# Kernel optimization log

Hardware: AMD Instinct MI355X
Metric: run time of the kernel (lower is better)

The kernel has to match this reference:

```python
import jax, jax.numpy as jnp
import numpy as np

N, E = 50000, 800000
F_IN, H, C = 128, 4, 32
NEG_SLOPE = 0.2

def setup_inputs() -> dict:
    key = jax.random.key(0)
    k1, k2, k3, k4, k5, k6 = jax.random.split(key, 6)
    x = jax.random.normal(k1, (N, F_IN), dtype=jnp.float32)
    edge_index = jax.random.randint(k2, (2, E), 0, N, dtype=jnp.int64)
    # GATConv params: lin weight [F_IN, H*C], att_src/att_dst [H, C], bias [H*C]
    W = jax.random.normal(k3, (F_IN, H * C), dtype=jnp.float32) * (1.0 / np.sqrt(F_IN))
    att_src = jax.random.normal(k4, (H, C), dtype=jnp.float32) * (1.0 / np.sqrt(C))
    att_dst = jax.random.normal(k5, (H, C), dtype=jnp.float32) * (1.0 / np.sqrt(C))
    bias = jax.random.normal(k6, (H * C,), dtype=jnp.float32) * 0.01
    return {"x": x, "edge_index": edge_index, "W": W, "att_src": att_src, "att_dst": att_dst, "bias": bias}

def reference(x, edge_index, W, att_src, att_dst, bias):
    # Linear transform: [N, H, C]
    h = (x @ W).reshape(N, H, C)
    # Per-node attention logits: [N, H]
    a_src = jnp.einsum('nhc,hc->nh', h, att_src)
    a_dst = jnp.einsum('nhc,hc->nh', h, att_dst)
    # PyG GATConv adds self-loops by default
    loop = jnp.arange(N, dtype=edge_index.dtype)
    src = jnp.concatenate([edge_index[0], loop])  # message source j
    dst = jnp.concatenate([edge_index[1], loop])  # message target i
    # Edge logits + LeakyReLU: [E+N, H]
    e = jax.nn.leaky_relu(a_src[src] + a_dst[dst], NEG_SLOPE)
    # Segment softmax over incoming edges per target node
    m = jax.ops.segment_max(e, dst, num_segments=N)  # [N, H]
    e_exp = jnp.exp(e - m[dst])
    denom = jax.ops.segment_sum(e_exp, dst, num_segments=N)  # [N, H]
    att = e_exp / denom[dst]  # [E+N, H]
    # Scatter-add weighted messages: [N, H, C]
    out = jax.ops.segment_sum(h[src] * att[:, :, None], dst, num_segments=N)
    return out.reshape(N, H * C) + bias
```

## Files before the change

### kernel.cpp

```cpp
#include <hip/hip_runtime.h>
#include <cstdint>

#define NNODES 50000
#define NEDGES 800000
#define NEG 0.2f
#define NBKT 196
#define BCAP 5120

typedef __attribute__((ext_vector_type(8))) short short8;
typedef __attribute__((ext_vector_type(4))) float f32x4;

#define AS_STRIDE 136
#define CS_STRIDE 132

__device__ __forceinline__ float leaky(float v) { return v > 0.f ? v : NEG * v; }

__device__ __forceinline__ unsigned short f2bf(float f) {
    unsigned int u = __float_as_uint(f);
    u += 0x7fff + ((u >> 16) & 1);
    return (unsigned short)(u >> 16);
}

__device__ __forceinline__ int block_excl_scan(int v, int t) {
    __shared__ int wsum[4];
    const int lane = t & 63, wv = t >> 6;
    int x = v;
    #pragma unroll
    for (int m = 1; m < 64; m <<= 1) {
        int u = __shfl_up(x, m);
        if (lane >= m) x += u;
    }
    if (lane == 63) wsum[wv] = x;
    __syncthreads();
    if (t == 0) {
        int run = 0;
        #pragma unroll
        for (int i = 0; i < 4; ++i) { int tmp = wsum[i]; wsum[i] = run; run += tmp; }
    }
    __syncthreads();
    return x - v + wsum[wv];
}

__global__ __launch_bounds__(256) void gemm_k(const float* __restrict__ x,
                                              const float* __restrict__ W,
                                              unsigned short* __restrict__ hb,
                                              const float* __restrict__ att_src,
                                              const float* __restrict__ att_dst,
                                              float* __restrict__ a_src,
                                              float* __restrict__ a_dst) {
    __shared__ __align__(16) char smem[52224];
    unsigned short* As = (unsigned short*)smem;
    unsigned short* Bs = (unsigned short*)(smem + 17408);
    float*          Cs = (float*)smem;

    const int tid = threadIdx.x;
    const int rbase = blockIdx.x * 64;

    #pragma unroll
    for (int i = 0; i < 8; ++i) {
        int f = tid + i * 256;
        int r = f >> 5, c4 = (f & 31) * 4;
        float4 xv = make_float4(0.f, 0.f, 0.f, 0.f);
        if (rbase + r < NNODES) xv = ((const float4*)x)[(size_t)(rbase + r) * 32 + (f & 31)];
        unsigned int p0 = ((unsigned int)f2bf(xv.y) << 16) | f2bf(xv.x);
        unsigned int p1 = ((unsigned int)f2bf(xv.w) << 16) | f2bf(xv.z);
        *(uint2*)(As + r * AS_STRIDE + c4) = make_uint2(p0, p1);
    }
    #pragma unroll
    for (int i = 0; i < 64; ++i) {
        int f = tid + i * 256;
        int k = f >> 7, n = f & 127;
        Bs[n * AS_STRIDE + k] = f2bf(W[f]);
    }
    __syncthreads();

    const int lane = tid & 63, w = tid >> 6;
    const int quad = lane >> 4, m16 = lane & 15;

    short8 af[4];
    #pragma unroll
    for (int s = 0; s < 4; ++s)
        af[s] = *(const short8*)(As + (w * 16 + m16) * AS_STRIDE + s * 32 + quad * 8);

    f32x4 acc[8];
    #pragma unroll
    for (int t = 0; t < 8; ++t) acc[t] = (f32x4){0.f, 0.f, 0.f, 0.f};

    #pragma unroll
    for (int t = 0; t < 8; ++t) {
        #pragma unroll
        for (int s = 0; s < 4; ++s) {
            short8 bf = *(const short8*)(Bs + (t * 16 + m16) * AS_STRIDE + s * 32 + quad * 8);
            acc[t] = __builtin_amdgcn_mfma_f32_16x16x32_bf16(af[s], bf, acc[t], 0, 0, 0);
        }
    }
    __syncthreads();

    #pragma unroll
    for (int t = 0; t < 8; ++t)
        #pragma unroll
        for (int r = 0; r < 4; ++r)
            Cs[(w * 16 + quad * 4 + r) * CS_STRIDE + t * 16 + m16] = acc[t][r];
    __syncthreads();

    const int cp = lane;
    float2 as_v = ((const float2*)att_src)[cp];
    float2 ad_v = ((const float2*)att_dst)[cp];
    #pragma unroll
    for (int r = 0; r < 16; ++r) {
        int row = w * 16 + r;
        int row_g = rbase + row;
        float2 cv = *(const float2*)(Cs + row * CS_STRIDE + 2 * cp);
        ushort2 hs;
        hs.x = f2bf(cv.x); hs.y = f2bf(cv.y);
        if (row_g < NNODES) ((ushort2*)(hb + (size_t)row_g * 128))[cp] = hs;
        float ps = cv.x * as_v.x + cv.y * as_v.y;
        float pd = cv.x * ad_v.x + cv.y * ad_v.y;
        #pragma unroll
        for (int m = 8; m >= 1; m >>= 1) {
            ps += __shfl_xor(ps, m, 16);
            pd += __shfl_xor(pd, m, 16);
        }
        if (row_g < NNODES && (cp & 15) == 0) {
            a_src[row_g * 4 + (cp >> 4)] = ps;
            a_dst[row_g * 4 + (cp >> 4)] = pd;
        }
    }
}

__global__ __launch_bounds__(256) void bin_k(const int* __restrict__ ei,
                                             int* __restrict__ bcnt,
                                             unsigned int* __restrict__ bktdata) {
    __shared__ int lhist[NBKT];
    __shared__ int lofs[NBKT];
    __shared__ int lcur[NBKT];
    __shared__ int gbase[NBKT];
    __shared__ unsigned int staged[4096];
    const int b = blockIdx.x, t = threadIdx.x;
    for (int i = t; i < NBKT; i += 256) lhist[i] = 0;
    __syncthreads();
    unsigned int pk[16];
    int bk[16];
    const int e0 = b * 4096;
    #pragma unroll
    for (int i = 0; i < 16; ++i) {
        int e = e0 + i * 256 + t;
        if (e < NEDGES) {
            int s = ei[e], d = ei[NEDGES + e];
            bk[i] = d >> 8;
            pk[i] = ((unsigned)bk[i] << 24) | ((unsigned)(d & 255) << 16) | (unsigned)s;
            atomicAdd(&lhist[bk[i]], 1);
        } else bk[i] = -1;
    }
    __syncthreads();
    int v = (t < NBKT) ? lhist[t] : 0;
    int excl = block_excl_scan(v, t);
    if (t < NBKT) { lofs[t] = excl; lcur[t] = excl; }
    __syncthreads();
    if (t < NBKT) gbase[t] = (v > 0) ? atomicAdd(&bcnt[t], v) : 0;
    #pragma unroll
    for (int i = 0; i < 16; ++i) {
        if (bk[i] >= 0) {
            int pos = atomicAdd(&lcur[bk[i]], 1);
            staged[pos] = pk[i];
        }
    }
    __syncthreads();
    const int total = lofs[NBKT - 1] + lhist[NBKT - 1];
    for (int i = t; i < total; i += 256) {
        unsigned int ent = staged[i];
        int bb = ent >> 24;
        int pos = gbase[bb] + (i - lofs[bb]);
        bktdata[(size_t)bb * BCAP + pos] = ent & 0x00FFFFFFu;
    }
}

__global__ __launch_bounds__(256) void bscan_k(const int* __restrict__ bcnt,
                                               int* __restrict__ bktoff) {
    const int t = threadIdx.x;
    int v = (t < NBKT) ? bcnt[t] : 0;
    int excl = block_excl_scan(v, t);
    if (t < NBKT) bktoff[t] = excl;
}

__global__ __launch_bounds__(256) void sort_k(const int* __restrict__ bcnt,
                                              const int* __restrict__ bktoff,
                                              const unsigned int* __restrict__ bktdata,
                                              int* __restrict__ off,
                                              int* __restrict__ csr) {
    __shared__ unsigned int staged[BCAP];
    __shared__ int sorted[BCAP];
    __shared__ int lcnt[256];
    __shared__ int lcur[256];
    const int b = blockIdx.x, t = threadIdx.x;
    const int cnt = bcnt[b], base = bktoff[b];
    lcnt[t] = 0;
    for (int i = t; i < cnt; i += 256) staged[i] = bktdata[(size_t)b * BCAP + i];
    __syncthreads();
    for (int i = t; i < cnt; i += 256) atomicAdd(&lcnt[staged[i] >> 16], 1);
    __syncthreads();
    int v = lcnt[t];
    int excl = block_excl_scan(v, t);
    lcur[t] = excl;
    const int node = b * 256 + t;
    if (node <= NNODES) off[node] = base + excl;
    __syncthreads();
    for (int i = t; i < cnt; i += 256) {
        unsigned int ent = staged[i];
        int pos = atomicAdd(&lcur[ent >> 16], 1);
        sorted[pos] = (int)(ent & 0xFFFFu);
    }
    __syncthreads();
    for (int i = t; i < cnt; i += 256) csr[base + i] = sorted[i];
}

__global__ __launch_bounds__(256) void gather_k(const int* __restrict__ off,
                                                const int* __restrict__ csr,
                                                const unsigned short* __restrict__ hb,
                                                const float* __restrict__ a_src,
                                                const float* __restrict__ a_dst,
                                                const float* __restrict__ bias,
                                                float* __restrict__ out) {
    const int wid = threadIdx.x >> 6, lane = threadIdx.x & 63;
    const int n = blockIdx.x * 4 + wid;
    if (n >= NNODES) return;
    const int head = lane >> 4;
    const int sub  = lane & 15;
    const int g = head, q = sub;
    const int head_c = q >> 2;

    const float a_d = a_dst[n * 4 + head];
    float acc[8];
    #pragma unroll
    for (int k = 0; k < 8; ++k) acc[k] = 0.f;

    if (g == 0) {
        float wsc = __expf(leaky(a_src[n * 4 + head_c] + a_dst[n * 4 + head_c]));
        uint4 hv = ((const uint4*)(hb + (size_t)n * 128))[q];
        acc[0] = wsc * __uint_as_float(hv.x << 16);
        acc[1] = wsc * __uint_as_float(hv.x & 0xffff0000u);
        acc[2] = wsc * __uint_as_float(hv.y << 16);
        acc[3] = wsc * __uint_as_float(hv.y & 0xffff0000u);
        acc[4] = wsc * __uint_as_float(hv.z << 16);
        acc[5] = wsc * __uint_as_float(hv.z & 0xffff0000u);
        acc[6] = wsc * __uint_as_float(hv.w << 16);
        acc[7] = wsc * __uint_as_float(hv.w & 0xffff0000u);
    }
    float denom = (sub == 0) ? __expf(leaky(a_src[n * 4 + head] + a_d)) : 0.f;

    const int beg = off[n], end = off[n + 1];
    for (int base = beg; base < end; base += 16) {
        int m = end - base; if (m > 16) m = 16;
        int s = 0;
        float w = 0.f;
        if (sub < m) {
            s = csr[base + sub];
            w = __expf(leaky(a_src[s * 4 + head] + a_d));
        }
        denom += w;
        #pragma unroll
        for (int jj = 0; jj < 4; ++jj) {
            int j = jj * 4 + g;
            int   sj = __shfl(s, j);
            float wj = __shfl(w, (head_c << 4) | j);
            if (j < m) {
                uint4 hv = ((const uint4*)(hb + (size_t)sj * 128))[q];
                acc[0] += wj * __uint_as_float(hv.x << 16);
                acc[1] += wj * __uint_as_float(hv.x & 0xffff0000u);
                acc[2] += wj * __uint_as_float(hv.y << 16);
                acc[3] += wj * __uint_as_float(hv.y & 0xffff0000u);
                acc[4] += wj * __uint_as_float(hv.z << 16);
                acc[5] += wj * __uint_as_float(hv.z & 0xffff0000u);
                acc[6] += wj * __uint_as_float(hv.w << 16);
                acc[7] += wj * __uint_as_float(hv.w & 0xffff0000u);
            }
        }
    }
    #pragma unroll
    for (int mm = 8; mm >= 1; mm >>= 1) denom += __shfl_xor(denom, mm, 16);
    const float inv = __frcp_rn(__shfl(denom, head_c << 4));
    #pragma unroll
    for (int k = 0; k < 8; ++k) {
        acc[k] += __shfl_xor(acc[k], 16);
        acc[k] += __shfl_xor(acc[k], 32);
    }
    if (g == 0) {
        float4 b0 = ((const float4*)bias)[2 * q];
        float4 b1 = ((const float4*)bias)[2 * q + 1];
        float4* orow = (float4*)(out + (size_t)n * 128);
        orow[2 * q]     = make_float4(acc[0] * inv + b0.x, acc[1] * inv + b0.y,
                                      acc[2] * inv + b0.z, acc[3] * inv + b0.w);
        orow[2 * q + 1] = make_float4(acc[4] * inv + b1.x, acc[5] * inv + b1.y,
                                      acc[6] * inv + b1.z, acc[7] * inv + b1.w);
    }
}

extern "C" void kernel_launch(void* const* d_in, const int* in_sizes, int n_in,
                              void* d_out, int out_size, void* d_ws, size_t ws_size,
                              hipStream_t stream) {
    const float* x     = (const float*)d_in[0];
    const int*   ei    = (const int*)d_in[1];
    const float* W     = (const float*)d_in[2];
    const float* att_s = (const float*)d_in[3];
    const float* att_d = (const float*)d_in[4];
    const float* bias  = (const float*)d_in[5];
    float*       out   = (float*)d_out;
    char*        ws    = (char*)d_ws;

    unsigned short* hb = (unsigned short*)(ws);
    float* a_src  = (float*)(ws + 12800000);
    float* a_dst  = (float*)(ws + 13600000);
    int*   off    = (int*)  (ws + 14400000);
    int*   csr    = (int*)  (ws + 14600768);
    unsigned int* bktdata = (unsigned int*)(ws + 17800768);
    int*   bcnt   = (int*)  (ws + 21814848);
    int*   bktoff = (int*)  (ws + 21815680);

    hipMemsetAsync(bcnt, 0, NBKT * sizeof(int), stream);
    gemm_k  <<<782,   256, 0, stream>>>(x, W, hb, att_s, att_d, a_src, a_dst);
    bin_k   <<<196,   256, 0, stream>>>(ei, bcnt, bktdata);
    bscan_k <<<1,     256, 0, stream>>>(bcnt, bktoff);
    sort_k  <<<196,   256, 0, stream>>>(bcnt, bktoff, bktdata, off, csr);
    gather_k<<<12500, 256, 0, stream>>>(off, csr, hb, a_src, a_dst, bias, out);
}
```

Baseline: 170.1 us.

## Merge GEMM and edge binning into one launch, fold bucket scan into sort

The GEMM and edge-binning kernels become a single launch whose blocks branch on block index, so the two independent stages run concurrently. The single-block bucket scan kernel is removed and each sort block recomputes the 196-entry prefix scan itself. The W load is also vectorised to float4. Together this cuts two kernel launches and the serialization between them. In exchange, binning blocks now reserve the GEMM's large shared allocation, which may lower their occupancy.

```diff
diff --git a/kernel.cpp b/kernel.cpp
--- a/kernel.cpp
+++ b/kernel.cpp
@@ -6,6 +6,7 @@
 #define NEG 0.2f
 #define NBKT 196
 #define BCAP 5120
+#define GEMM_BLOCKS 782
 
 typedef __attribute__((ext_vector_type(8))) short short8;
 typedef __attribute__((ext_vector_type(4))) float f32x4;
@@ -41,150 +42,146 @@
     return x - v + wsum[wv];
 }
 
-__global__ __launch_bounds__(256) void gemm_k(const float* __restrict__ x,
-                                              const float* __restrict__ W,
-                                              unsigned short* __restrict__ hb,
-                                              const float* __restrict__ att_src,
-                                              const float* __restrict__ att_dst,
-                                              float* __restrict__ a_src,
-                                              float* __restrict__ a_dst) {
+__global__ __launch_bounds__(256) void fused_k(const float* __restrict__ x,
+                                               const float* __restrict__ W,
+                                               unsigned short* __restrict__ hb,
+                                               const float* __restrict__ att_src,
+                                               const float* __restrict__ att_dst,
+                                               float* __restrict__ a_src,
+                                               float* __restrict__ a_dst,
+                                               const int* __restrict__ ei,
+                                               int* __restrict__ bcnt,
+                                               unsigned int* __restrict__ bktdata) {
     __shared__ __align__(16) char smem[52224];
-    unsigned short* As = (unsigned short*)smem;
-    unsigned short* Bs = (unsigned short*)(smem + 17408);
-    float*          Cs = (float*)smem;
-
     const int tid = threadIdx.x;
-    const int rbase = blockIdx.x * 64;
-
-    #pragma unroll
-    for (int i = 0; i < 8; ++i) {
-        int f = tid + i * 256;
-        int r = f >> 5, c4 = (f & 31) * 4;
-        float4 xv = make_float4(0.f, 0.f, 0.f, 0.f);
-        if (rbase + r < NNODES) xv = ((const float4*)x)[(size_t)(rbase + r) * 32 + (f & 31)];
-        unsigned int p0 = ((unsigned int)f2bf(xv.y) << 16) | f2bf(xv.x);
-        unsigned int p1 = ((unsigned int)f2bf(xv.w) << 16) | f2bf(xv.z);
-        *(uint2*)(As + r * AS_STRIDE + c4) = make_uint2(p0, p1);
-    }
-    #pragma unroll
-    for (int i = 0; i < 64; ++i) {
-        int f = tid + i * 256;
-        int k = f >> 7, n = f & 127;
-        Bs[n * AS_STRIDE + k] = f2bf(W[f]);
-    }
-    __syncthreads();
-
-    const int lane = tid & 63, w = tid >> 6;
-    const int quad = lane >> 4, m16 = lane & 15;
-
-    short8 af[4];
-    #pragma unroll
-    for (int s = 0; s < 4; ++s)
-        af[s] = *(const short8*)(As + (w * 16 + m16) * AS_STRIDE + s * 32 + quad * 8);
-
-    f32x4 acc[8];
-    #pragma unroll
-    for (int t = 0; t < 8; ++t) acc[t] = (f32x4){0.f, 0.f, 0.f, 0.f};
-
-    #pragma unroll
-    for (int t = 0; t < 8; ++t) {
-        #pragma unroll
-        for (int s = 0; s < 4; ++s) {
-            short8 bf = *(const short8*)(Bs + (t * 16 + m16) * AS_STRIDE + s * 32 + quad * 8);
-            acc[t] = __builtin_amdgcn_mfma_f32_16x16x32_bf16(af[s], bf, acc[t], 0, 0, 0);
-        }
-    }
-    __syncthreads();
-
-    #pragma unroll
-    for (int t = 0; t < 8; ++t)
-        #pragma unroll
-        for (int r = 0; r < 4; ++r)
-            Cs[(w * 16 + quad * 4 + r) * CS_STRIDE + t * 16 + m16] = acc[t][r];
-    __syncthreads();
-
-    const int cp = lane;
-    float2 as_v = ((const float2*)att_src)[cp];
-    float2 ad_v = ((const float2*)att_dst)[cp];
-    #pragma unroll
-    for (int r = 0; r < 16; ++r) {
-        int row = w * 16 + r;
-        int row_g = rbase + row;
-        float2 cv = *(const float2*)(Cs + row * CS_STRIDE + 2 * cp);
-        ushort2 hs;
-        hs.x = f2bf(cv.x); hs.y = f2bf(cv.y);
-        if (row_g < NNODES) ((ushort2*)(hb + (size_t)row_g * 128))[cp] = hs;
-        float ps = cv.x * as_v.x + cv.y * as_v.y;
-        float pd = cv.x * ad_v.x + cv.y * ad_v.y;
-        #pragma unroll
-        for (int m = 8; m >= 1; m >>= 1) {
-            ps += __shfl_xor(ps, m, 16);
-            pd += __shfl_xor(pd, m, 16);
-        }
-        if (row_g < NNODES && (cp & 15) == 0) {
-            a_src[row_g * 4 + (cp >> 4)] = ps;
-            a_dst[row_g * 4 + (cp >> 4)] = pd;
-        }
-    }
-}
-
-__global__ __launch_bounds__(256) void bin_k(const int* __restrict__ ei,
-                                             int* __restrict__ bcnt,
-                                             unsigned int* __restrict__ bktdata) {
-    __shared__ int lhist[NBKT];
-    __shared__ int lofs[NBKT];
-    __shared__ int lcur[NBKT];
-    __shared__ int gbase[NBKT];
-    __shared__ unsigned int staged[4096];
-    const int b = blockIdx.x, t = threadIdx.x;
-    for (int i = t; i < NBKT; i += 256) lhist[i] = 0;
-    __syncthreads();
-    unsigned int pk[16];
-    int bk[16];
-    const int e0 = b * 4096;
-    #pragma unroll
-    for (int i = 0; i < 16; ++i) {
-        int e = e0 + i * 256 + t;
-        if (e < NEDGES) {
-            int s = ei[e], d = ei[NEDGES + e];
-            bk[i] = d >> 8;
-            pk[i] = ((unsigned)bk[i] << 24) | ((unsigned)(d & 255) << 16) | (unsigned)s;
-            atomicAdd(&lhist[bk[i]], 1);
-        } else bk[i] = -1;
-    }
-    __syncthreads();
-    int v = (t < NBKT) ? lhist[t] : 0;
-    int excl = block_excl_scan(v, t);
-    if (t < NBKT) { lofs[t] = excl; lcur[t] = excl; }
-    __syncthreads();
-    if (t < NBKT) gbase[t] = (v > 0) ? atomicAdd(&bcnt[t], v) : 0;
-    #pragma unroll
-    for (int i = 0; i < 16; ++i) {
-        if (bk[i] >= 0) {
-            int pos = atomicAdd(&lcur[bk[i]], 1);
-            staged[pos] = pk[i];
-        }
-    }
-    __syncthreads();
-    const int total = lofs[NBKT - 1] + lhist[NBKT - 1];
-    for (int i = t; i < total; i += 256) {
-        unsigned int ent = staged[i];
-        int bb = ent >> 24;
-        int pos = gbase[bb] + (i - lofs[bb]);
-        bktdata[(size_t)bb * BCAP + pos] = ent & 0x00FFFFFFu;
-    }
-}
-
-__global__ __launch_bounds__(256) void bscan_k(const int* __restrict__ bcnt,
-                                               int* __restrict__ bktoff) {
-    const int t = threadIdx.x;
-    int v = (t < NBKT) ? bcnt[t] : 0;
-    int excl = block_excl_scan(v, t);
-    if (t < NBKT) bktoff[t] = excl;
+
+    if (blockIdx.x < GEMM_BLOCKS) {
+        unsigned short* As = (unsigned short*)smem;
+        unsigned short* Bs = (unsigned short*)(smem + 17408);
+        float*          Cs = (float*)smem;
+        const int rbase = blockIdx.x * 64;
+
+        #pragma unroll
+        for (int i = 0; i < 8; ++i) {
+            int f = tid + i * 256;
+            int r = f >> 5, c4 = (f & 31) * 4;
+            float4 xv = make_float4(0.f, 0.f, 0.f, 0.f);
+            if (rbase + r < NNODES) xv = ((const float4*)x)[(size_t)(rbase + r) * 32 + (f & 31)];
+            unsigned int p0 = ((unsigned int)f2bf(xv.y) << 16) | f2bf(xv.x);
+            unsigned int p1 = ((unsigned int)f2bf(xv.w) << 16) | f2bf(xv.z);
+            *(uint2*)(As + r * AS_STRIDE + c4) = make_uint2(p0, p1);
+        }
+        #pragma unroll
+        for (int i = 0; i < 16; ++i) {
+            int f4 = tid + i * 256;
+            int k = f4 >> 5, n4 = (f4 & 31) * 4;
+            float4 wv = ((const float4*)W)[f4];
+            Bs[(n4 + 0) * AS_STRIDE + k] = f2bf(wv.x);
+            Bs[(n4 + 1) * AS_STRIDE + k] = f2bf(wv.y);
+            Bs[(n4 + 2) * AS_STRIDE + k] = f2bf(wv.z);
+            Bs[(n4 + 3) * AS_STRIDE + k] = f2bf(wv.w);
+        }
+        __syncthreads();
+
+        const int lane = tid & 63, w = tid >> 6;
+        const int quad = lane >> 4, m16 = lane & 15;
+
+        short8 af[4];
+        #pragma unroll
+        for (int s = 0; s < 4; ++s)
+            af[s] = *(const short8*)(As + (w * 16 + m16) * AS_STRIDE + s * 32 + quad * 8);
+
+        f32x4 acc[8];
+        #pragma unroll
+        for (int t = 0; t < 8; ++t) acc[t] = (f32x4){0.f, 0.f, 0.f, 0.f};
+
+        #pragma unroll
+        for (int t = 0; t < 8; ++t) {
+            #pragma unroll
+            for (int s = 0; s < 4; ++s) {
+                short8 bf = *(const short8*)(Bs + (t * 16 + m16) * AS_STRIDE + s * 32 + quad * 8);
+                acc[t] = __builtin_amdgcn_mfma_f32_16x16x32_bf16(af[s], bf, acc[t], 0, 0, 0);
+            }
+        }
+        __syncthreads();
+
+        #pragma unroll
+        for (int t = 0; t < 8; ++t)
+            #pragma unroll
+            for (int r = 0; r < 4; ++r)
+                Cs[(w * 16 + quad * 4 + r) * CS_STRIDE + t * 16 + m16] = acc[t][r];
+        __syncthreads();
+
+        const int cp = lane;
+        float2 as_v = ((const float2*)att_src)[cp];
+        float2 ad_v = ((const float2*)att_dst)[cp];
+        #pragma unroll
+        for (int r = 0; r < 16; ++r) {
+            int row = w * 16 + r;
+            int row_g = rbase + row;
+            float2 cv = *(const float2*)(Cs + row * CS_STRIDE + 2 * cp);
+            ushort2 hs;
+            hs.x = f2bf(cv.x); hs.y = f2bf(cv.y);
+            if (row_g < NNODES) ((ushort2*)(hb + (size_t)row_g * 128))[cp] = hs;
+            float ps = cv.x * as_v.x + cv.y * as_v.y;
+            float pd = cv.x * ad_v.x + cv.y * ad_v.y;
+            #pragma unroll
+            for (int m = 8; m >= 1; m >>= 1) {
+                ps += __shfl_xor(ps, m, 16);
+                pd += __shfl_xor(pd, m, 16);
+            }
+            if (row_g < NNODES && (cp & 15) == 0) {
+                a_src[row_g * 4 + (cp >> 4)] = ps;
+                a_dst[row_g * 4 + (cp >> 4)] = pd;
+            }
+        }
+    } else {
+        int* lhist = (int*)smem;
+        int* lofs  = lhist + NBKT;
+        int* lcur  = lofs + NBKT;
+        int* gbase = lcur + NBKT;
+        unsigned int* staged = (unsigned int*)(gbase + NBKT);
+        const int b = blockIdx.x - GEMM_BLOCKS, t = tid;
+        for (int i = t; i < NBKT; i += 256) lhist[i] = 0;
+        __syncthreads();
+        unsigned int pk[16];
+        int bk[16];
+        const int e0 = b * 4096;
+        #pragma unroll
+        for (int i = 0; i < 16; ++i) {
+            int e = e0 + i * 256 + t;
+            if (e < NEDGES) {
+                int s = ei[e], d = ei[NEDGES + e];
+                bk[i] = d >> 8;
+                pk[i] = ((unsigned)bk[i] << 24) | ((unsigned)(d & 255) << 16) | (unsigned)s;
+                atomicAdd(&lhist[bk[i]], 1);
+            } else bk[i] = -1;
+        }
+        __syncthreads();
+        int v = (t < NBKT) ? lhist[t] : 0;
+        int excl = block_excl_scan(v, t);
+        if (t < NBKT) { lofs[t] = excl; lcur[t] = excl; }
+        __syncthreads();
+        if (t < NBKT) gbase[t] = (v > 0) ? atomicAdd(&bcnt[t], v) : 0;
+        #pragma unroll
+        for (int i = 0; i < 16; ++i) {
+            if (bk[i] >= 0) {
+                int pos = atomicAdd(&lcur[bk[i]], 1);
+                staged[pos] = pk[i];
+            }
+        }
+        __syncthreads();
+        const int total = lofs[NBKT - 1] + lhist[NBKT - 1];
+        for (int i = t; i < total; i += 256) {
+            unsigned int ent = staged[i];
+            int bb = ent >> 24;
+            int pos = gbase[bb] + (i - lofs[bb]);
+            bktdata[(size_t)bb * BCAP + pos] = ent & 0x00FFFFFFu;
+        }
+    }
 }
 
 __global__ __launch_bounds__(256) void sort_k(const int* __restrict__ bcnt,
-                                              const int* __restrict__ bktoff,
                                               const unsigned int* __restrict__ bktdata,
                                               int* __restrict__ off,
                                               int* __restrict__ csr) {
@@ -192,8 +189,13 @@
     __shared__ int sorted[BCAP];
     __shared__ int lcnt[256];
     __shared__ int lcur[256];
+    __shared__ int sbase, scnt;
     const int b = blockIdx.x, t = threadIdx.x;
-    const int cnt = bcnt[b], base = bktoff[b];
+    int bv = (t < NBKT) ? bcnt[t] : 0;
+    int bexcl = block_excl_scan(bv, t);
+    if (t == b) { sbase = bexcl; scnt = bv; }
+    __syncthreads();
+    const int cnt = scnt, base = sbase;
     lcnt[t] = 0;
     for (int i = t; i < cnt; i += 256) staged[i] = bktdata[(size_t)b * BCAP + i];
     __syncthreads();
@@ -314,12 +316,10 @@
     int*   csr    = (int*)  (ws + 14600768);
     unsigned int* bktdata = (unsigned int*)(ws + 17800768);
     int*   bcnt   = (int*)  (ws + 21814848);
-    int*   bktoff = (int*)  (ws + 21815680);
 
     hipMemsetAsync(bcnt, 0, NBKT * sizeof(int), stream);
-    gemm_k  <<<782,   256, 0, stream>>>(x, W, hb, att_s, att_d, a_src, a_dst);
-    bin_k   <<<196,   256, 0, stream>>>(ei, bcnt, bktdata);
-    bscan_k <<<1,     256, 0, stream>>>(bcnt, bktoff);
-    sort_k  <<<196,   256, 0, stream>>>(bcnt, bktoff, bktdata, off, csr);
+    fused_k <<<GEMM_BLOCKS + NBKT, 256, 0, stream>>>(x, W, hb, att_s, att_d,
+                                                     a_src, a_dst, ei, bcnt, bktdata);
+    sort_k  <<<NBKT,  256, 0, stream>>>(bcnt, bktdata, off, csr);
     gather_k<<<12500, 256, 0, stream>>>(off, csr, hb, a_src, a_dst, bias, out);
 }
```

Result: faster. 163.8 us (-3.7%).
